# Optimization experiments

Measured on AMD Instinct MI355X. Metric: run time of the kernel, lower is better.

The kernel has to match this reference:

```python
import jax, jax.numpy as jnp
import numpy as np

N_NODES = 50000
N_EDGES = 600000
IN_FEAT = 128
EDGE_DIM = 3
N_HEADS = 4
OUT_FEAT = 32  # per head; N_HEADS*OUT_FEAT == IN_FEAT -> residual_proj is Identity


def setup_inputs() -> dict:
    key = jax.random.key(0)
    ks = jax.random.split(key, 16)
    s = 0.05
    H, F = N_HEADS, OUT_FEAT
    return {
        "node_feats": jax.random.normal(ks[0], (N_NODES, IN_FEAT), jnp.float32),
        "edge_feat": jax.random.normal(ks[1], (N_EDGES, EDGE_DIM), jnp.float32),
        "src": jax.random.randint(ks[2], (N_EDGES,), 0, N_NODES),
        "dst": jax.random.randint(ks[3], (N_EDGES,), 0, N_NODES),
        "W_em1": jax.random.normal(ks[4], (EDGE_DIM, 2 * EDGE_DIM), jnp.float32) * s,
        "b_em1": jnp.zeros((2 * EDGE_DIM,), jnp.float32),
        "W_em2": jax.random.normal(ks[5], (2 * EDGE_DIM, EDGE_DIM), jnp.float32) * s,
        "b_em2": jnp.zeros((EDGE_DIM,), jnp.float32),
        "W_np": jax.random.normal(ks[6], (IN_FEAT, IN_FEAT), jnp.float32) * s,
        "b_np": jnp.zeros((IN_FEAT,), jnp.float32),
        "W_fc": jax.random.normal(ks[7], (IN_FEAT + EDGE_DIM, H * F), jnp.float32) * s,
        "attn_l": jax.random.normal(ks[8], (H, F), jnp.float32) * s,
        "attn_r": jax.random.normal(ks[9], (H, F), jnp.float32) * s,
        "gat_bias": jnp.zeros((H * F,), jnp.float32),
        "ln_gamma": jnp.ones((H * F,), jnp.float32),
        "ln_beta": jnp.zeros((H * F,), jnp.float32),
    }


def reference(node_feats, edge_feat, src, dst, W_em1, b_em1, W_em2, b_em2,
              W_np, b_np, W_fc, attn_l, attn_r, gat_bias, ln_gamma, ln_beta):
    N = node_feats.shape[0]
    H, F = attn_l.shape
    # edge MLP: Linear -> SiLU -> Linear
    e = jax.nn.silu(edge_feat @ W_em1 + b_em1) @ W_em2 + b_em2            # [E, ED]
    p = node_feats @ W_np + b_np                                          # [N, IN]
    src_in = jnp.concatenate([p[src], e], axis=1)                         # [E, IN+ED]
    dst_in = jnp.concatenate([p[dst], e], axis=1)                         # [E, IN+ED]
    temp = jnp.zeros((N, src_in.shape[1]), node_feats.dtype)
    temp = temp.at[src].add(src_in).at[dst].add(dst_in)                   # scatter_add x2
    # GATConv (eval mode: feat_drop/attn_drop are identity)
    h = (temp @ W_fc).reshape(N, H, F)                                    # [N, H, F]
    el = jnp.einsum('nhf,hf->nh', h, attn_l)                              # [N, H]
    er = jnp.einsum('nhf,hf->nh', h, attn_r)                              # [N, H]
    logits = jax.nn.leaky_relu(el[src] + er[dst], negative_slope=0.2)     # [E, H]
    # destination-wise edge softmax (stable)
    m = jax.ops.segment_max(logits, dst, num_segments=N)                  # [N, H]
    a = jnp.exp(logits - m[dst])                                          # [E, H]
    z = jax.ops.segment_sum(a, dst, num_segments=N)                       # [N, H]
    alpha = a / z[dst]                                                    # [E, H]
    msg = alpha[:, :, None] * h[src]                                      # [E, H, F]
    rst = jax.ops.segment_sum(msg, dst, num_segments=N)                   # [N, H, F]
    rst = rst + gat_bias.reshape(1, H, F)
    gat_out = rst.reshape(N, H * F)
    out = gat_out + node_feats                                            # residual (Identity proj)
    mu = out.mean(axis=-1, keepdims=True)
    var = out.var(axis=-1, keepdims=True)
    out = (out - mu) / jnp.sqrt(var + 1e-5) * ln_gamma + ln_beta          # LayerNorm
    return jax.nn.silu(out)
```

## Files before the change

### kernel.cpp

```cpp
#include <hip/hip_runtime.h>
#include <hip/hip_bf16.h>

#define IN_FEAT 128
#define N_HEADS 4
#define OUT_FEAT 32

typedef __attribute__((ext_vector_type(8))) short short8;
typedef __attribute__((ext_vector_type(4))) float floatx4;

__device__ __forceinline__ void bf16split(float x, short& hi, short& lo) {
    unsigned u = __float_as_uint(x);
    unsigned r = (u + 0x7FFFu + ((u >> 16) & 1u)) & 0xFFFF0000u;
    hi = (short)(r >> 16);
    float res = x - __uint_as_float(r);
    unsigned u2 = __float_as_uint(res);
    unsigned r2 = u2 + 0x7FFFu + ((u2 >> 16) & 1u);
    lo = (short)(r2 >> 16);
}

__device__ __forceinline__ unsigned short bf16rne(float x) {
    unsigned u = __float_as_uint(x);
    return (unsigned short)((u + 0x7FFFu + ((u >> 16) & 1u)) >> 16);
}

__global__ void edge_scatter_kernel(const float* __restrict__ ef,
                                    const int* __restrict__ src, const int* __restrict__ dst,
                                    const float* __restrict__ W1, const float* __restrict__ b1,
                                    const float* __restrict__ W2, const float* __restrict__ b2,
                                    float* __restrict__ nd, int* __restrict__ erank, int E) {
    int t = blockIdx.x * blockDim.x + threadIdx.x;
    int e = t >> 3;
    int sub = t & 7;
    if (e >= E) return;
    float x0 = ef[e * 3 + 0], x1 = ef[e * 3 + 1], x2 = ef[e * 3 + 2];
    float hbuf[6];
#pragma unroll
    for (int j = 0; j < 6; j++) {
        float v = x0 * W1[0 * 6 + j] + x1 * W1[1 * 6 + j] + x2 * W1[2 * 6 + j] + b1[j];
        hbuf[j] = v / (1.0f + __expf(-v));
    }
    int j = sub & 3;
    float val;
    if (j == 0) {
        val = 1.0f;
    } else {
        float v = b2[j - 1];
#pragma unroll
        for (int k = 0; k < 6; k++) v += hbuf[k] * W2[k * 3 + (j - 1)];
        val = v;
    }
    int side = sub >> 2;
    int node = side ? dst[e] : src[e];
    int slot = (side && j == 0) ? 4 : j;
    float old = atomicAdd(&nd[(size_t)node * 8 + slot], val);
    if (sub == 4) erank[e] = (int)old;
}

__global__ __launch_bounds__(1024) void scan1_kernel(const float* __restrict__ nd,
                                                     int* __restrict__ excl,
                                                     int* __restrict__ bsum, int N) {
    __shared__ int buf[1024];
    int t = threadIdx.x;
    int i = blockIdx.x * 1024 + t;
    int v = (i < N) ? (int)nd[(size_t)i * 8 + 4] : 0;
    buf[t] = v;
    __syncthreads();
    for (int d = 1; d < 1024; d <<= 1) {
        int x = (t >= d) ? buf[t - d] : 0;
        __syncthreads();
        buf[t] += x;
        __syncthreads();
    }
    if (i < N) excl[i] = buf[t] - v;
    if (t == 1023) bsum[blockIdx.x] = buf[1023];
}

__global__ __launch_bounds__(1024) void scan3_kernel(const int* __restrict__ excl,
                                                     const int* __restrict__ bsum,
                                                     int* __restrict__ off, int N, int E) {
    __shared__ int base;
    if (threadIdx.x == 0) {
        int s = 0;
        for (int k = 0; k < (int)blockIdx.x; k++) s += bsum[k];
        base = s;
    }
    __syncthreads();
    int i = blockIdx.x * 1024 + threadIdx.x;
    if (i < N) off[i] = excl[i] + base;
    if (i == 0) off[N] = E;
}

__global__ void wcomb_kernel(const float* __restrict__ W_np, const float* __restrict__ W_fc,
                             const float* __restrict__ b_np,
                             short* __restrict__ WBh, short* __restrict__ WBl,
                             float* __restrict__ bvec,
                             float4* __restrict__ ndz, int zcnt) {
    for (int i = blockIdx.x * blockDim.x + threadIdx.x; i < zcnt; i += gridDim.x * blockDim.x)
        ndz[i] = (float4){0.f, 0.f, 0.f, 0.f};

    int i = blockIdx.x;
    int o = threadIdx.x;
    float acc = 0.0f;
    for (int j = 0; j < 128; j++) acc += W_np[i * 128 + j] * W_fc[j * 128 + o];
    short hi, lo;
    bf16split(acc, hi, lo);
    int t    = o >> 4;
    int kk   = i >> 5;
    int lane = ((i >> 3) & 3) * 16 + (o & 15);
    int jj   = i & 7;
    int fi = ((t * 4 + kk) * 64 + lane) * 8 + jj;
    WBh[fi] = hi;
    WBl[fi] = lo;
    if (i == 0) {
        float bb = 0.0f;
        for (int j = 0; j < 128; j++) bb += b_np[j] * W_fc[j * 128 + o];
        bvec[o] = bb;
    }
}

__global__ __launch_bounds__(256) void binh_kernel(
        const int* __restrict__ src, const int* __restrict__ dst,
        const int* __restrict__ eoff, const int* __restrict__ erank,
        int* __restrict__ ssrc, int E,
        const float* __restrict__ nf,
        const short* __restrict__ WBh, const short* __restrict__ WBl,
        const float* __restrict__ bvec, const float* __restrict__ W_fc,
        const float* __restrict__ nd,
        const float* __restrict__ attn_l, const float* __restrict__ attn_r,
        unsigned short* __restrict__ h16,
        float* __restrict__ el, float* __restrict__ er, int N) {
    __shared__ short lWh[16384];
    __shared__ short lWl[16384];
    {
        const int4* s1 = (const int4*)WBh;
        const int4* s2 = (const int4*)WBl;
        int4* d1 = (int4*)lWh;
        int4* d2 = (int4*)lWl;
        for (int i = threadIdx.x; i < 2048; i += 256) { d1[i] = s1[i]; d2[i] = s2[i]; }
    }
    __syncthreads();

    {
        int stride = gridDim.x * 256;
        for (int e = blockIdx.x * 256 + threadIdx.x; e < E; e += stride) {
            ssrc[eoff[dst[e]] + erank[e]] = src[e];
        }
    }

    const int w = threadIdx.x >> 6, l = threadIdx.x & 63;
    const int lrow = l & 15, lhalf = l >> 4;
    const int n0 = blockIdx.x * 64 + w * 16;
    const int arow = n0 + lrow;

    short8 ah[4];
#pragma unroll
    for (int kk = 0; kk < 4; kk++) {
        float v[8];
        if (arow < N) {
            const float* p = &nf[(size_t)arow * 128 + kk * 32 + lhalf * 8];
            float4 f0 = *(const float4*)p;
            float4 f1 = *(const float4*)(p + 4);
            v[0] = f0.x; v[1] = f0.y; v[2] = f0.z; v[3] = f0.w;
            v[4] = f1.x; v[5] = f1.y; v[6] = f1.z; v[7] = f1.w;
        } else {
#pragma unroll
            for (int j = 0; j < 8; j++) v[j] = 0.0f;
        }
#pragma unroll
        for (int j = 0; j < 8; j++) ah[kk][j] = (short)bf16rne(v[j]);
    }

    floatx4 acc[8];
#pragma unroll
    for (int t = 0; t < 8; t++) acc[t] = (floatx4){0.f, 0.f, 0.f, 0.f};
#pragma unroll
    for (int t = 0; t < 8; t++) {
#pragma unroll
        for (int kk = 0; kk < 4; kk++) {
            int fi = ((t * 4 + kk) * 64 + l) * 8;
            short8 bh = *(const short8*)&lWh[fi];
            short8 bl = *(const short8*)&lWl[fi];
            acc[t] = __builtin_amdgcn_mfma_f32_16x16x32_bf16(ah[kk], bh, acc[t], 0, 0, 0);
            acc[t] = __builtin_amdgcn_mfma_f32_16x16x32_bf16(ah[kk], bl, acc[t], 0, 0, 0);
        }
    }

    float bv[8], w0[8], w1[8], w2[8], alb[8], arb[8];
#pragma unroll
    for (int t = 0; t < 8; t++) {
        int o = t * 16 + lrow;
        bv[t] = bvec[o];
        w0[t] = W_fc[128 * 128 + o];
        w1[t] = W_fc[129 * 128 + o];
        w2[t] = W_fc[130 * 128 + o];
        alb[t] = attn_l[o];
        arb[t] = attn_r[o];
    }
#pragma unroll
    for (int r = 0; r < 4; r++) {
        int node = n0 + lhalf * 4 + r;
        bool valid = node < N;
        float dg = 0.f, e0 = 0.f, e1 = 0.f, e2 = 0.f;
        if (valid) {
            dg = nd[(size_t)node * 8 + 0] + nd[(size_t)node * 8 + 4];
            e0 = nd[(size_t)node * 8 + 1];
            e1 = nd[(size_t)node * 8 + 2];
            e2 = nd[(size_t)node * 8 + 3];
        }
        float pl[4] = {0.f, 0.f, 0.f, 0.f}, pr[4] = {0.f, 0.f, 0.f, 0.f};
#pragma unroll
        for (int t = 0; t < 8; t++) {
            float hv = dg * (acc[t][r] + bv[t]) + e0 * w0[t] + e1 * w1[t] + e2 * w2[t];
            if (valid) h16[(size_t)node * 128 + t * 16 + lrow] = bf16rne(hv);
            pl[t >> 1] += hv * alb[t];
            pr[t >> 1] += hv * arb[t];
        }
#pragma unroll
        for (int hd = 0; hd < 4; hd++) {
#pragma unroll
            for (int mask = 1; mask <= 8; mask <<= 1) {
                pl[hd] += __shfl_xor(pl[hd], mask);
                pr[hd] += __shfl_xor(pr[hd], mask);
            }
        }
        if (valid) {
            if (lrow < 4)      el[node * 4 + lrow]       = pl[lrow];
            else if (lrow < 8) er[node * 4 + (lrow - 4)] = pr[lrow - 4];
        }
    }
}

__global__ __launch_bounds__(256) void gather_kernel(
        const int* __restrict__ off, const int* __restrict__ sorted_src,
        const float* __restrict__ el, const float* __restrict__ er,
        const unsigned short* __restrict__ h16, const float* __restrict__ nf,
        const float* __restrict__ gat_bias, const float* __restrict__ gamma,
        const float* __restrict__ beta, float* __restrict__ out, int N) {
    int wid  = (blockIdx.x * blockDim.x + threadIdx.x) >> 6;
    int lane = threadIdx.x & 63;
    int half = lane >> 5;
    int li   = lane & 31;
    int n = wid * 2 + half;
    if (n >= N) return;
    int o0 = li * 4;
    int hd = li >> 3;
    float ern = er[(unsigned)(n * 4 + hd)];
    int beg = off[n], end = off[n + 1];
    float z = 0.f, a0 = 0.f, a1 = 0.f, a2 = 0.f, a3 = 0.f;
    int j = beg;
    if ((end - beg) & 1) {
        int s = sorted_src[j++];
        float l = el[(unsigned)(s * 4 + hd)] + ern;
        l = (l > 0.f) ? l : 0.2f * l;
        float p = __expf(l);
        uint2 hb = *(const uint2*)&h16[(unsigned)(s * 128 + o0)];
        z  = p;
        a0 = p * __uint_as_float(hb.x << 16);
        a1 = p * __uint_as_float(hb.x & 0xFFFF0000u);
        a2 = p * __uint_as_float(hb.y << 16);
        a3 = p * __uint_as_float(hb.y & 0xFFFF0000u);
    }
    for (; j < end; j += 2) {
        int sA = sorted_src[j];
        int sB = sorted_src[j + 1];
        float elA = el[(unsigned)(sA * 4 + hd)];
        float elB = el[(unsigned)(sB * 4 + hd)];
        uint2 hA = *(const uint2*)&h16[(unsigned)(sA * 128 + o0)];
        uint2 hB = *(const uint2*)&h16[(unsigned)(sB * 128 + o0)];
        float lA = elA + ern; lA = (lA > 0.f) ? lA : 0.2f * lA;
        float lB = elB + ern; lB = (lB > 0.f) ? lB : 0.2f * lB;
        float pA = __expf(lA);
        float pB = __expf(lB);
        z  += pA + pB;
        a0 += pA * __uint_as_float(hA.x << 16)         + pB * __uint_as_float(hB.x << 16);
        a1 += pA * __uint_as_float(hA.x & 0xFFFF0000u) + pB * __uint_as_float(hB.x & 0xFFFF0000u);
        a2 += pA * __uint_as_float(hA.y << 16)         + pB * __uint_as_float(hB.y << 16);
        a3 += pA * __uint_as_float(hA.y & 0xFFFF0000u) + pB * __uint_as_float(hB.y & 0xFFFF0000u);
    }
    float izv = (end > beg) ? 1.0f / z : 0.f;
    float4 nfv = *(const float4*)&nf[(size_t)n * 128 + o0];
    float v0 = a0 * izv + gat_bias[o0]     + nfv.x;
    float v1 = a1 * izv + gat_bias[o0 + 1] + nfv.y;
    float v2 = a2 * izv + gat_bias[o0 + 2] + nfv.z;
    float v3 = a3 * izv + gat_bias[o0 + 3] + nfv.w;
    float s  = v0 + v1 + v2 + v3;
    float s2 = v0 * v0 + v1 * v1 + v2 * v2 + v3 * v3;
#pragma unroll
    for (int mask = 1; mask <= 16; mask <<= 1) {
        s  += __shfl_xor(s, mask);
        s2 += __shfl_xor(s2, mask);
    }
    float mu = s * (1.0f / 128.0f);
    float var = s2 * (1.0f / 128.0f) - mu * mu;
    float inv = rsqrtf(var + 1e-5f);
    float y0 = (v0 - mu) * inv * gamma[o0]     + beta[o0];
    float y1 = (v1 - mu) * inv * gamma[o0 + 1] + beta[o0 + 1];
    float y2 = (v2 - mu) * inv * gamma[o0 + 2] + beta[o0 + 2];
    float y3 = (v3 - mu) * inv * gamma[o0 + 3] + beta[o0 + 3];
    float4 ov;
    ov.x = y0 / (1.0f + __expf(-y0));
    ov.y = y1 / (1.0f + __expf(-y1));
    ov.z = y2 / (1.0f + __expf(-y2));
    ov.w = y3 / (1.0f + __expf(-y3));
    *(float4*)&out[(size_t)n * 128 + o0] = ov;
}

extern "C" void kernel_launch(void* const* d_in, const int* in_sizes, int n_in,
                              void* d_out, int out_size, void* d_ws, size_t ws_size,
                              hipStream_t stream) {
    const float* nf     = (const float*)d_in[0];
    const float* ef     = (const float*)d_in[1];
    const int*   src    = (const int*)d_in[2];
    const int*   dst    = (const int*)d_in[3];
    const float* W_em1  = (const float*)d_in[4];
    const float* b_em1  = (const float*)d_in[5];
    const float* W_em2  = (const float*)d_in[6];
    const float* b_em2  = (const float*)d_in[7];
    const float* W_np   = (const float*)d_in[8];
    const float* b_np   = (const float*)d_in[9];
    const float* W_fc   = (const float*)d_in[10];
    const float* attn_l = (const float*)d_in[11];
    const float* attn_r = (const float*)d_in[12];
    const float* g_bias = (const float*)d_in[13];
    const float* ln_g   = (const float*)d_in[14];
    const float* ln_b   = (const float*)d_in[15];

    const int N = in_sizes[0] / IN_FEAT;
    const int E = in_sizes[2];

    float* ws = (float*)d_ws;
    size_t off_w = 0;
    auto alloc = [&](size_t nelem) {
        float* p = ws + off_w;
        off_w += (nelem + 63) & ~(size_t)63;
        return p;
    };
    float* nd    = alloc((size_t)N * 8);
    short* WBh   = (short*)alloc(128 * 128 / 2);
    short* WBl   = (short*)alloc(128 * 128 / 2);
    float* bvec  = alloc(128);
    unsigned short* h16 = (unsigned short*)alloc((size_t)N * 64);
    float* el    = alloc((size_t)N * 4);
    float* er    = alloc((size_t)N * 4);
    int*   erank  = (int*)alloc(E);
    int*   eoff   = (int*)alloc(N + 1);
    int*   ssrc   = (int*)alloc(E);
    int*   excl   = (int*)alloc(N);
    int*   bsum   = (int*)alloc(1024);

    const int nb = (N + 1023) / 1024;

    wcomb_kernel<<<128, 128, 0, stream>>>(W_np, W_fc, b_np, WBh, WBl, bvec,
                                          (float4*)nd, N * 2);
    edge_scatter_kernel<<<((size_t)E * 8 + 255) / 256, 256, 0, stream>>>(
        ef, src, dst, W_em1, b_em1, W_em2, b_em2, nd, erank, E);
    scan1_kernel<<<nb, 1024, 0, stream>>>(nd, excl, bsum, N);
    scan3_kernel<<<nb, 1024, 0, stream>>>(excl, bsum, eoff, N, E);
    binh_kernel<<<(N + 63) / 64, 256, 0, stream>>>(src, dst, eoff, erank, ssrc, E,
                                                   nf, WBh, WBl, bvec, W_fc, nd,
                                                   attn_l, attn_r, h16, el, er, N);
    gather_kernel<<<((size_t)N * 32 + 255) / 256, 256, 0, stream>>>(eoff, ssrc, el, er, h16, nf,
                                                                    g_bias, ln_g, ln_b,
                                                                    (float*)d_out, N);
}
```

Baseline: 148.5 us.

## Privatize node scatter accumulators per XCC to use workgroup-scope atomics

The edge scatter now writes into eight per-XCC copies of the node accumulator array, chosen by reading the hardware XCC id, and uses relaxed workgroup-scope atomics. The aim is to keep atomics in the local L2 and avoid device-scope coherence traffic across chiplets. The scan and binh kernels then reduce the eight copies, and a per-node per-XCC base table rebuilds each edge's rank for the CSR placement. In exchange it zeroes and reads eight times more accumulator memory and adds a cbase8 table. Correctness depends on every block on a given XCC sharing that XCC's L2, so that workgroup-scope atomics from different CUs still combine correctly.

```diff
diff --git a/kernel.cpp b/kernel.cpp
--- a/kernel.cpp
+++ b/kernel.cpp
@@ -23,15 +23,24 @@
     return (unsigned short)((u + 0x7FFFu + ((u >> 16) & 1u)) >> 16);
 }
 
+__device__ __forceinline__ int xcc_id() {
+    unsigned x;
+    asm volatile("s_getreg_b32 %0, hwreg(HW_REG_XCC_ID)" : "=s"(x));
+    return (int)(x & 7u);
+}
+
 __global__ void edge_scatter_kernel(const float* __restrict__ ef,
                                     const int* __restrict__ src, const int* __restrict__ dst,
                                     const float* __restrict__ W1, const float* __restrict__ b1,
                                     const float* __restrict__ W2, const float* __restrict__ b2,
-                                    float* __restrict__ nd, int* __restrict__ erank, int E) {
+                                    float* __restrict__ nd8, size_t ndStride,
+                                    int* __restrict__ erank, int E) {
     int t = blockIdx.x * blockDim.x + threadIdx.x;
     int e = t >> 3;
     int sub = t & 7;
     if (e >= E) return;
+    int c = xcc_id();
+    float* ndc = nd8 + (size_t)c * ndStride;
     float x0 = ef[e * 3 + 0], x1 = ef[e * 3 + 1], x2 = ef[e * 3 + 2];
     float hbuf[6];
 #pragma unroll
@@ -52,17 +61,28 @@
     int side = sub >> 2;
     int node = side ? dst[e] : src[e];
     int slot = (side && j == 0) ? 4 : j;
-    float old = atomicAdd(&nd[(size_t)node * 8 + slot], val);
-    if (sub == 4) erank[e] = (int)old;
-}
-
-__global__ __launch_bounds__(1024) void scan1_kernel(const float* __restrict__ nd,
+    float old = __hip_atomic_fetch_add(&ndc[(size_t)node * 8 + slot], val,
+                                       __ATOMIC_RELAXED, __HIP_MEMORY_SCOPE_WORKGROUP);
+    if (sub == 4) erank[e] = ((int)old) | (c << 24);
+}
+
+__global__ __launch_bounds__(1024) void scan1_kernel(const float* __restrict__ nd8, size_t ndStride,
+                                                     int* __restrict__ cbase8,
                                                      int* __restrict__ excl,
                                                      int* __restrict__ bsum, int N) {
     __shared__ int buf[1024];
     int t = threadIdx.x;
     int i = blockIdx.x * 1024 + t;
-    int v = (i < N) ? (int)nd[(size_t)i * 8 + 4] : 0;
+    int v = 0;
+    if (i < N) {
+        int s = 0;
+#pragma unroll
+        for (int c = 0; c < 8; c++) {
+            cbase8[i * 8 + c] = s;
+            s += (int)nd8[(size_t)c * ndStride + (size_t)i * 8 + 4];
+        }
+        v = s;
+    }
     buf[t] = v;
     __syncthreads();
     for (int d = 1; d < 1024; d <<= 1) {
@@ -121,11 +141,12 @@
 __global__ __launch_bounds__(256) void binh_kernel(
         const int* __restrict__ src, const int* __restrict__ dst,
         const int* __restrict__ eoff, const int* __restrict__ erank,
+        const int* __restrict__ cbase8,
         int* __restrict__ ssrc, int E,
         const float* __restrict__ nf,
         const short* __restrict__ WBh, const short* __restrict__ WBl,
         const float* __restrict__ bvec, const float* __restrict__ W_fc,
-        const float* __restrict__ nd,
+        const float* __restrict__ nd8, size_t ndStride,
         const float* __restrict__ attn_l, const float* __restrict__ attn_r,
         unsigned short* __restrict__ h16,
         float* __restrict__ el, float* __restrict__ er, int N) {
@@ -143,7 +164,11 @@
     {
         int stride = gridDim.x * 256;
         for (int e = blockIdx.x * 256 + threadIdx.x; e < E; e += stride) {
-            ssrc[eoff[dst[e]] + erank[e]] = src[e];
+            int d  = dst[e];
+            int er_ = erank[e];
+            int c  = er_ >> 24;
+            int rk = er_ & 0x00FFFFFF;
+            ssrc[eoff[d] + cbase8[d * 8 + c] + rk] = src[e];
         }
     }
 
@@ -202,10 +227,14 @@
         bool valid = node < N;
         float dg = 0.f, e0 = 0.f, e1 = 0.f, e2 = 0.f;
         if (valid) {
-            dg = nd[(size_t)node * 8 + 0] + nd[(size_t)node * 8 + 4];
-            e0 = nd[(size_t)node * 8 + 1];
-            e1 = nd[(size_t)node * 8 + 2];
-            e2 = nd[(size_t)node * 8 + 3];
+#pragma unroll
+            for (int c = 0; c < 8; c++) {
+                const float* p = nd8 + (size_t)c * ndStride + (size_t)node * 8;
+                dg += p[0] + p[4];
+                e0 += p[1];
+                e1 += p[2];
+                e2 += p[3];
+            }
         }
         float pl[4] = {0.f, 0.f, 0.f, 0.f}, pr[4] = {0.f, 0.f, 0.f, 0.f};
 #pragma unroll
@@ -335,7 +364,8 @@
         off_w += (nelem + 63) & ~(size_t)63;
         return p;
     };
-    float* nd    = alloc((size_t)N * 8);
+    const size_t ndStride = (size_t)N * 8;
+    float* nd8   = alloc(ndStride * 8);
     short* WBh   = (short*)alloc(128 * 128 / 2);
     short* WBl   = (short*)alloc(128 * 128 / 2);
     float* bvec  = alloc(128);
@@ -344,6 +374,7 @@
     float* er    = alloc((size_t)N * 4);
     int*   erank  = (int*)alloc(E);
     int*   eoff   = (int*)alloc(N + 1);
+    int*   cbase8 = (int*)alloc((size_t)N * 8);
     int*   ssrc   = (int*)alloc(E);
     int*   excl   = (int*)alloc(N);
     int*   bsum   = (int*)alloc(1024);
@@ -351,13 +382,13 @@
     const int nb = (N + 1023) / 1024;
 
     wcomb_kernel<<<128, 128, 0, stream>>>(W_np, W_fc, b_np, WBh, WBl, bvec,
-                                          (float4*)nd, N * 2);
+                                          (float4*)nd8, N * 16);
     edge_scatter_kernel<<<((size_t)E * 8 + 255) / 256, 256, 0, stream>>>(
-        ef, src, dst, W_em1, b_em1, W_em2, b_em2, nd, erank, E);
-    scan1_kernel<<<nb, 1024, 0, stream>>>(nd, excl, bsum, N);
+        ef, src, dst, W_em1, b_em1, W_em2, b_em2, nd8, ndStride, erank, E);
+    scan1_kernel<<<nb, 1024, 0, stream>>>(nd8, ndStride, cbase8, excl, bsum, N);
     scan3_kernel<<<nb, 1024, 0, stream>>>(excl, bsum, eoff, N, E);
-    binh_kernel<<<(N + 63) / 64, 256, 0, stream>>>(src, dst, eoff, erank, ssrc, E,
-                                                   nf, WBh, WBl, bvec, W_fc, nd,
+    binh_kernel<<<(N + 63) / 64, 256, 0, stream>>>(src, dst, eoff, erank, cbase8, ssrc, E,
+                                                   nf, WBh, WBl, bvec, W_fc, nd8, ndStride,
                                                    attn_l, attn_r, h16, el, er, N);
     gather_kernel<<<((size_t)N * 32 + 255) / 256, 256, 0, stream>>>(eoff, ssrc, el, er, h16, nf,
                                                                     g_bias, ln_g, ln_b,
```

New measurement: 161.3 us. 1.09x slower.
